# Kernel tuning notes

Measured on AMD Instinct MI355X. Metric: run time of the kernel, lower is better.

The kernel has to match this reference:

```python
import jax, jax.numpy as jnp
import numpy as np
import math

B, D, T, R = 32, 512, 64, 49
K = 64
OUT = 1024


def setup_inputs() -> dict:
    key = jax.random.key(0)
    k_x, k_c, k_w = jax.random.split(key, 3)
    x = jax.random.normal(k_x, (B, D, T, R), dtype=jnp.float32)
    mask = jnp.ones((B, T), dtype=jnp.int32)
    centroids = jax.random.normal(k_c, (K, D), dtype=jnp.float32) / math.sqrt(D)
    conv_w = centroids  # reset_parameters() copies centroids into the 1x1 conv weight
    red_w = jax.random.normal(k_w, (OUT, K * D), dtype=jnp.float32) / math.sqrt(K * D)
    ln_gamma = jnp.ones((OUT,), dtype=jnp.float32)
    ln_beta = jnp.zeros((OUT,), dtype=jnp.float32)
    return {"x": x, "mask": mask, "centroids": centroids, "conv_w": conv_w,
            "red_w": red_w, "ln_gamma": ln_gamma, "ln_beta": ln_beta}


def _l2norm(v, axis):
    n = jnp.sqrt(jnp.sum(v * v, axis=axis, keepdims=True))
    return v / jnp.maximum(n, 1e-12)


def reference(x, mask, centroids, conv_w, red_w, ln_gamma, ln_beta):
    b, d, t, r = x.shape
    # 1x1 conv == contraction over channel dim: [b,k,t,r]
    logits = jnp.einsum('bdtr,kd->bktr', x, conv_w)
    assign = jax.nn.softmax(logits, axis=1)
    # mask applied to residual*assign == masking the assignments
    m = mask.astype(x.dtype)[:, None, :, None]          # [b,1,t,1]
    assign = assign * m
    a_sum = jnp.sum(assign, axis=(2, 3))                 # [b,k]
    # vlad[b,k,d] = sum_{t,r} a[b,k,t,r]*x[b,d,t,r] - a_sum[b,k]*c[k,d]
    vlad = jnp.einsum('bktr,bdtr->bkd', assign, x) - a_sum[:, :, None] * centroids[None]
    vlad = _l2norm(vlad, axis=2)                         # intra-normalization
    vlad = vlad.reshape(b, -1)                           # [b, K*D]
    vlad = _l2norm(vlad, axis=1)
    vlad = vlad @ red_w.T                                # [b, OUT]
    # LayerNorm (eps=1e-5)
    mu = jnp.mean(vlad, axis=-1, keepdims=True)
    var = jnp.mean((vlad - mu) ** 2, axis=-1, keepdims=True)
    return (vlad - mu) / jnp.sqrt(var + 1e-5) * ln_gamma + ln_beta
```

## Files before the change

kernel.cpp:

```cpp
#include <hip/hip_runtime.h>
#include <math.h>

#define BB 32
#define DD 512
#define TT 64
#define RR 49
#define TR 3136
#define KK 64
#define OUTN 1024
#define KD 32768

typedef float f4 __attribute__((ext_vector_type(4)));
typedef short s8 __attribute__((ext_vector_type(8)));

#define OFF_ASSIGN 0ull
#define OFF_VLADP  12845056ull
#define OFF_VN     21233664ull
#define OFF_SS     23330816ull
#define OFF_ASUM   23339008ull
#define OFF_Y      23347200ull

__device__ __forceinline__ unsigned long long pack4(float a, float b, float c, float d) {
    union { float f; unsigned u; } A, B, C, D;
    A.f = a; B.f = b; C.f = c; D.f = d;
    unsigned lo = __builtin_amdgcn_perm(B.u + 0x8000u, A.u + 0x8000u, 0x07060302u);
    unsigned hi = __builtin_amdgcn_perm(D.u + 0x8000u, C.u + 0x8000u, 0x07060302u);
    return (unsigned long long)lo | ((unsigned long long)hi << 32);
}

__global__ __launch_bounds__(256) void kA(const float* __restrict__ x,
                                          const int* __restrict__ mask,
                                          const float* __restrict__ convw,
                                          unsigned short* __restrict__ assign,
                                          float* __restrict__ asum) {
    __shared__ unsigned short cw_l[64 * 136];
    __shared__ unsigned short xT_l[64 * 136];
    __shared__ float sm[64 * 68];

    const int blk = blockIdx.x;
    const int b = blk / 49;
    const int pc = blk % 49;
    const int p0 = pc * 64;
    const int tid = threadIdx.x;
    const int lane = tid & 63;
    const int wv = tid >> 6;
    const int quad = lane >> 4;
    const int l15 = lane & 15;

    f4 acc[4];
#pragma unroll
    for (int t = 0; t < 4; ++t) acc[t] = (f4){0.f, 0.f, 0.f, 0.f};

    const float* xb = x + (size_t)b * DD * TR;

    for (int dc = 0; dc < 4; ++dc) {
        const int d0 = dc * 128;
        __syncthreads();
#pragma unroll
        for (int i = 0; i < 8; ++i) {
            int lin = i * 256 + tid;
            int row = lin >> 5;
            int c = lin & 31;
            f4 v = *(const f4*)(convw + row * DD + d0 + c * 4);
            *(unsigned long long*)(cw_l + row * 136 + c * 4) = pack4(v[0], v[1], v[2], v[3]);
        }
#pragma unroll
        for (int i = 0; i < 2; ++i) {
            int lin = i * 256 + tid;
            int dq = lin >> 4;
            int pq = lin & 15;
            const float* xp = xb + (size_t)(d0 + dq * 4) * TR + p0 + pq * 4;
            f4 a0 = *(const f4*)(xp);
            f4 a1 = *(const f4*)(xp + TR);
            f4 a2 = *(const f4*)(xp + 2 * TR);
            f4 a3 = *(const f4*)(xp + 3 * TR);
#pragma unroll
            for (int jj = 0; jj < 4; ++jj) {
                int j = (jj + pq) & 3;
                *(unsigned long long*)(xT_l + (pq * 4 + j) * 136 + dq * 4) =
                    pack4(a0[j], a1[j], a2[j], a3[j]);
            }
        }
        __syncthreads();
#pragma unroll
        for (int ks = 0; ks < 4; ++ks) {
            int off = ks * 32 + quad * 8;
            s8 af = *(const s8*)(cw_l + (wv * 16 + l15) * 136 + off);
#pragma unroll
            for (int t = 0; t < 4; ++t) {
                s8 bfr = *(const s8*)(xT_l + (t * 16 + l15) * 136 + off);
                acc[t] = __builtin_amdgcn_mfma_f32_16x16x32_bf16(af, bfr, acc[t], 0, 0, 0);
            }
        }
    }
    __syncthreads();
#pragma unroll
    for (int t = 0; t < 4; ++t)
#pragma unroll
        for (int r = 0; r < 4; ++r)
            sm[(wv * 16 + quad * 4 + r) * 68 + t * 16 + l15] = acc[t][r];
    __syncthreads();

    float* redM = (float*)cw_l;
    float* redS = ((float*)cw_l) + 256;
    const int p = lane;
    float mx = -1e30f;
#pragma unroll
    for (int i = 0; i < 16; ++i) mx = fmaxf(mx, sm[(wv * 16 + i) * 68 + p]);
    redM[wv * 64 + p] = mx;
    __syncthreads();
    mx = fmaxf(fmaxf(redM[p], redM[64 + p]), fmaxf(redM[128 + p], redM[192 + p]));
    float s = 0.f;
#pragma unroll
    for (int i = 0; i < 16; ++i) {
        float e = __expf(sm[(wv * 16 + i) * 68 + p] - mx);
        sm[(wv * 16 + i) * 68 + p] = e;
        s += e;
    }
    redS[wv * 64 + p] = s;
    __syncthreads();
    float tot = redS[p] + redS[64 + p] + redS[128 + p] + redS[192 + p];
    const int tt = (p0 + p) / RR;
    const float inv = (float)mask[b * TT + tt] / tot;
#pragma unroll
    for (int i = 0; i < 16; ++i) {
        float v = sm[(wv * 16 + i) * 68 + p] * inv;
        sm[(wv * 16 + i) * 68 + p] = v;
        float r = v;
#pragma unroll
        for (int off = 32; off > 0; off >>= 1) r += __shfl_down(r, off, 64);
        if (lane == 0) atomicAdd(&asum[b * 64 + wv * 16 + i], r);
    }
    __syncthreads();
#pragma unroll
    for (int i = 0; i < 4; ++i) {
        int lin = i * 256 + tid;
        int kr = lin >> 4;
        int pq = lin & 15;
        f4 v = *(const f4*)(sm + kr * 68 + pq * 4);
        *(unsigned long long*)(assign + (size_t)(b * 64 + kr) * TR + p0 + pq * 4) =
            pack4(v[0], v[1], v[2], v[3]);
    }
}

__global__ __launch_bounds__(256) void kB(const float* __restrict__ x,
                                          const unsigned short* __restrict__ assign,
                                          const float* __restrict__ asum,
                                          const float* __restrict__ cent,
                                          float* __restrict__ vladP) {
    __shared__ unsigned short as_l[64 * 72];
    __shared__ unsigned short x_l[64 * 72];

    const int blk = blockIdx.x;
    const int b = blk >> 4;
    const int ds = (blk >> 1) & 7;
    const int ph = blk & 1;
    const int d0 = ds * 64;
    const int tid = threadIdx.x;
    const int lane = tid & 63;
    const int wv = tid >> 6;
    const int quad = lane >> 4;
    const int l15 = lane & 15;

    f4 acc[4];
#pragma unroll
    for (int t = 0; t < 4; ++t) acc[t] = (f4){0.f, 0.f, 0.f, 0.f};

    const int pcs = ph ? 25 : 0;
    const int pce = ph ? 49 : 25;
    for (int pc = pcs; pc < pce; ++pc) {
        const int p0 = pc * 64;
        __syncthreads();
#pragma unroll
        for (int i = 0; i < 2; ++i) {
            int lin = i * 256 + tid;
            int row = lin >> 3;
            int c = lin & 7;
            *(s8*)(as_l + row * 72 + c * 8) =
                *(const s8*)(assign + (size_t)(b * 64 + row) * TR + p0 + c * 8);
        }
#pragma unroll
        for (int i = 0; i < 4; ++i) {
            int lin = i * 256 + tid;
            int row = lin >> 4;
            int c = lin & 15;
            f4 v = *(const f4*)(x + (size_t)(b * DD + d0 + row) * TR + p0 + c * 4);
            *(unsigned long long*)(x_l + row * 72 + c * 4) = pack4(v[0], v[1], v[2], v[3]);
        }
        __syncthreads();
#pragma unroll
        for (int ks = 0; ks < 2; ++ks) {
            int off = ks * 32 + quad * 8;
            s8 af = *(const s8*)(as_l + (wv * 16 + l15) * 72 + off);
#pragma unroll
            for (int t = 0; t < 4; ++t) {
                s8 bfr = *(const s8*)(x_l + (t * 16 + l15) * 72 + off);
                acc[t] = __builtin_amdgcn_mfma_f32_16x16x32_bf16(af, bfr, acc[t], 0, 0, 0);
            }
        }
    }
    float* vp = vladP + (size_t)ph * (BB * KK * DD);
#pragma unroll
    for (int r = 0; r < 4; ++r) {
        const int k = wv * 16 + quad * 4 + r;
        float corr = ph ? 0.f : asum[b * 64 + k];
#pragma unroll
        for (int t = 0; t < 4; ++t) {
            const int d = d0 + t * 16 + l15;
            float v = acc[t][r];
            if (!ph) v -= corr * cent[k * DD + d];
            vp[(size_t)(b * 64 + k) * DD + d] = v;
        }
    }
}

__global__ __launch_bounds__(256) void kC1(const float* __restrict__ vladP,
                                           float* __restrict__ ss) {
    const int blk = blockIdx.x;
    const int b = blk >> 3;
    const int ks = blk & 7;
    const int tid = threadIdx.x;
    const int kr = tid >> 5;
    const int l32 = tid & 31;
    const int k = ks * 8 + kr;
    const float* q0 = vladP + (size_t)(b * 64 + k) * DD;
    const float* q1 = q0 + (size_t)BB * KK * DD;
    float s = 0.f;
#pragma unroll
    for (int i = 0; i < 4; ++i) {
        f4 a = *(const f4*)(q0 + i * 128 + l32 * 4);
        f4 c = *(const f4*)(q1 + i * 128 + l32 * 4);
#pragma unroll
        for (int j = 0; j < 4; ++j) { float v = a[j] + c[j]; s = fmaf(v, v, s); }
    }
    for (int off = 16; off > 0; off >>= 1) s += __shfl_down(s, off, 32);
    if (l32 == 0) ss[b * 64 + k] = s;
}

__global__ __launch_bounds__(256) void kC2(const float* __restrict__ vladP,
                                           const float* __restrict__ ss,
                                           unsigned short* __restrict__ vn) {
    __shared__ float sc[64];
    const int blk = blockIdx.x;
    const int b = blk >> 3;
    const int js = blk & 7;
    const int tid = threadIdx.x;
    if (tid < 64) {
        float rn = sqrtf(ss[b * 64 + tid]);
        float inv = 1.f / fmaxf(rn, 1e-12f);
        float cb = rn * inv; cb = cb * cb;
        float g = cb;
        for (int off = 32; off > 0; off >>= 1) g += __shfl_down(g, off, 64);
        g = __shfl(g, 0, 64);
        float gi = 1.f / fmaxf(sqrtf(g), 1e-12f);
        sc[tid] = inv * gi;
    }
    __syncthreads();
    const float* q0 = vladP + (size_t)b * KD;
    const float* q1 = q0 + (size_t)BB * KD;
#pragma unroll
    for (int it = 0; it < 4; ++it) {
        int j = js * 4096 + it * 1024 + tid * 4;
        f4 a = *(const f4*)(q0 + j);
        f4 c = *(const f4*)(q1 + j);
        float scl = sc[j >> 9];
        *(unsigned long long*)(vn + (size_t)b * KD + j) =
            pack4((a[0] + c[0]) * scl, (a[1] + c[1]) * scl,
                  (a[2] + c[2]) * scl, (a[3] + c[3]) * scl);
    }
}

__global__ __launch_bounds__(256) void kD(const unsigned short* __restrict__ vn,
                                          const float* __restrict__ redw,
                                          float* __restrict__ y) {
    __shared__ unsigned short rw_l[64 * 264];
    __shared__ unsigned short vl_l[32 * 264];

    const int blk = blockIdx.x;
    const int ot = blk & 15;
    const int js = blk >> 4;
    const int o0 = ot * 64;
    const int jb = js * 2048;
    const int tid = threadIdx.x;
    const int lane = tid & 63;
    const int wv = tid >> 6;
    const int quad = lane >> 4;
    const int l15 = lane & 15;

    f4 acc[2];
    acc[0] = (f4){0.f, 0.f, 0.f, 0.f};
    acc[1] = (f4){0.f, 0.f, 0.f, 0.f};

    for (int jc = 0; jc < 8; ++jc) {
        const int j0 = jb + jc * 256;
        __syncthreads();
#pragma unroll
        for (int i = 0; i < 16; ++i) {
            int lin = i * 256 + tid;
            int row = lin >> 6;
            int c = lin & 63;
            f4 v = *(const f4*)(redw + (size_t)(o0 + row) * KD + j0 + c * 4);
            *(unsigned long long*)(rw_l + row * 264 + c * 4) = pack4(v[0], v[1], v[2], v[3]);
        }
#pragma unroll
        for (int i = 0; i < 4; ++i) {
            int lin = i * 256 + tid;
            int row = lin >> 5;
            int c = lin & 31;
            *(s8*)(vl_l + row * 264 + c * 8) =
                *(const s8*)(vn + (size_t)row * KD + j0 + c * 8);
        }
        __syncthreads();
#pragma unroll
        for (int ks = 0; ks < 8; ++ks) {
            int off = ks * 32 + quad * 8;
            s8 bfr = *(const s8*)(rw_l + (wv * 16 + l15) * 264 + off);
#pragma unroll
            for (int t = 0; t < 2; ++t) {
                s8 af = *(const s8*)(vl_l + (t * 16 + l15) * 264 + off);
                acc[t] = __builtin_amdgcn_mfma_f32_16x16x32_bf16(af, bfr, acc[t], 0, 0, 0);
            }
        }
    }
#pragma unroll
    for (int t = 0; t < 2; ++t)
#pragma unroll
        for (int r = 0; r < 4; ++r) {
            int bq = t * 16 + quad * 4 + r;
            int o = o0 + wv * 16 + l15;
            atomicAdd(&y[(size_t)bq * OUTN + o], acc[t][r]);
        }
}

__global__ __launch_bounds__(256) void kE(const float* __restrict__ y,
                                          const float* __restrict__ gamma,
                                          const float* __restrict__ beta,
                                          float* __restrict__ out) {
    __shared__ float s1s[4], s2s[4];
    __shared__ float mu_s, rstd_s;

    const int b = blockIdx.x;
    const int tid = threadIdx.x;
    const int wave = tid >> 6;
    const int lane = tid & 63;

    f4 v = *(const f4*)(y + (size_t)b * OUTN + tid * 4);
    float s1 = v[0] + v[1] + v[2] + v[3];
    float s2 = v[0] * v[0] + v[1] * v[1] + v[2] * v[2] + v[3] * v[3];
    for (int off = 32; off > 0; off >>= 1) {
        s1 += __shfl_down(s1, off, 64);
        s2 += __shfl_down(s2, off, 64);
    }
    if (lane == 0) { s1s[wave] = s1; s2s[wave] = s2; }
    __syncthreads();
    if (tid == 0) {
        float S1 = s1s[0] + s1s[1] + s1s[2] + s1s[3];
        float S2 = s2s[0] + s2s[1] + s2s[2] + s2s[3];
        float mu = S1 / (float)OUTN;
        float var = S2 / (float)OUTN - mu * mu;
        mu_s = mu;
        rstd_s = 1.0f / sqrtf(var + 1e-5f);
    }
    __syncthreads();
    const float mu = mu_s, rstd = rstd_s;
    f4 g = *(const f4*)(gamma + tid * 4);
    f4 be = *(const f4*)(beta + tid * 4);
    f4 o;
#pragma unroll
    for (int i = 0; i < 4; ++i) o[i] = (v[i] - mu) * rstd * g[i] + be[i];
    *(f4*)(out + (size_t)b * OUTN + tid * 4) = o;
}

extern "C" void kernel_launch(void* const* d_in, const int* in_sizes, int n_in,
                              void* d_out, int out_size, void* d_ws, size_t ws_size,
                              hipStream_t stream) {
    const float* x     = (const float*)d_in[0];
    const int*   mask  = (const int*)d_in[1];
    const float* cent  = (const float*)d_in[2];
    const float* convw = (const float*)d_in[3];
    const float* redw  = (const float*)d_in[4];
    const float* gam   = (const float*)d_in[5];
    const float* bet   = (const float*)d_in[6];
    float* out = (float*)d_out;
    char* w = (char*)d_ws;

    unsigned short* assign = (unsigned short*)(w + OFF_ASSIGN);
    float*          vladP  = (float*)(w + OFF_VLADP);
    unsigned short* vn     = (unsigned short*)(w + OFF_VN);
    float*          ss     = (float*)(w + OFF_SS);
    float*          asum   = (float*)(w + OFF_ASUM);
    float*          y      = (float*)(w + OFF_Y);

    hipMemsetAsync(asum, 0, 64 * BB * sizeof(float), stream);
    hipMemsetAsync(y, 0, BB * OUTN * sizeof(float), stream);

    kA<<<BB * 49, 256, 0, stream>>>(x, mask, convw, assign, asum);
    kB<<<BB * 8 * 2, 256, 0, stream>>>(x, assign, asum, cent, vladP);
    kC1<<<BB * 8, 256, 0, stream>>>(vladP, ss);
    kC2<<<BB * 8, 256, 0, stream>>>(vladP, ss, vn);
    kD<<<16 * 16, 256, 0, stream>>>(vn, redw, y);
    kE<<<BB, 256, 0, stream>>>(y, gam, bet, out);
}
```

Measured before the change: 480.9 us.

## Pre-convert conv weights, double-buffer kA, register-prefetch kB/kD, widen split grids

Adds a small kernel that converts the conv weight to bf16 once, so kA loads A fragments straight from global memory instead of re-converting them into LDS in every block. kA now double-buffers the transposed x tile in LDS and prefetches the next chunk into registers while MFMAs run. kB and kD use register prefetch of the next tile. kB splits the pixel range 4 ways instead of 2, and kD splits K into 32 slices instead of 16, both to put more blocks in flight, at the cost of more partial sums and more atomics. The workspace layout is enlarged for four vlad partials and the bf16 weight buffer.

```diff
diff --git a/kernel.cpp b/kernel.cpp
--- a/kernel.cpp
+++ b/kernel.cpp
@@ -9,16 +9,18 @@
 #define KK 64
 #define OUTN 1024
 #define KD 32768
+#define PSTR 1048576ull
 
 typedef float f4 __attribute__((ext_vector_type(4)));
 typedef short s8 __attribute__((ext_vector_type(8)));
 
 #define OFF_ASSIGN 0ull
 #define OFF_VLADP  12845056ull
-#define OFF_VN     21233664ull
-#define OFF_SS     23330816ull
-#define OFF_ASUM   23339008ull
-#define OFF_Y      23347200ull
+#define OFF_VN     29622272ull
+#define OFF_CWB    31719424ull
+#define OFF_SS     31784960ull
+#define OFF_ASUM   31793152ull
+#define OFF_Y      31801344ull
 
 __device__ __forceinline__ unsigned long long pack4(float a, float b, float c, float d) {
     union { float f; unsigned u; } A, B, C, D;
@@ -28,14 +30,24 @@
     return (unsigned long long)lo | ((unsigned long long)hi << 32);
 }
 
+__global__ __launch_bounds__(256) void kW(const float* __restrict__ convw,
+                                          unsigned short* __restrict__ cwb) {
+    int idx = blockIdx.x * 256 + threadIdx.x;
+    f4 v = *(const f4*)(convw + idx * 4);
+    *(unsigned long long*)(cwb + idx * 4) = pack4(v[0], v[1], v[2], v[3]);
+}
+
 __global__ __launch_bounds__(256) void kA(const float* __restrict__ x,
                                           const int* __restrict__ mask,
-                                          const float* __restrict__ convw,
+                                          const unsigned short* __restrict__ cwb,
                                           unsigned short* __restrict__ assign,
                                           float* __restrict__ asum) {
-    __shared__ unsigned short cw_l[64 * 136];
-    __shared__ unsigned short xT_l[64 * 136];
-    __shared__ float sm[64 * 68];
+    __shared__ __align__(16) char smem[2 * 17408 + 2048];
+    unsigned short* xT0 = (unsigned short*)smem;
+    unsigned short* xT1 = (unsigned short*)(smem + 17408);
+    float* sm   = (float*)smem;
+    float* redM = (float*)(smem + 34816);
+    float* redS = redM + 256;
 
     const int blk = blockIdx.x;
     const int b = blk / 49;
@@ -46,54 +58,75 @@
     const int wv = tid >> 6;
     const int quad = lane >> 4;
     const int l15 = lane & 15;
-
+    const int pq = tid & 15;
+    const int dq0 = tid >> 4;
+
+    const float* xb = x + (size_t)b * DD * TR + p0 + pq * 4;
+    const unsigned short* cwrow = cwb + (wv * 16 + l15) * DD + quad * 8;
+
+    f4 xr[2][4];
+    s8 afc[4], afn[4];
     f4 acc[4];
 #pragma unroll
     for (int t = 0; t < 4; ++t) acc[t] = (f4){0.f, 0.f, 0.f, 0.f};
 
-    const float* xb = x + (size_t)b * DD * TR;
-
+    auto XLOAD = [&](int d0) {
+#pragma unroll
+        for (int i = 0; i < 2; ++i) {
+            const float* xp = xb + (size_t)(d0 + (dq0 + 16 * i) * 4) * TR;
+            xr[i][0] = *(const f4*)(xp);
+            xr[i][1] = *(const f4*)(xp + TR);
+            xr[i][2] = *(const f4*)(xp + 2 * TR);
+            xr[i][3] = *(const f4*)(xp + 3 * TR);
+        }
+    };
+    auto XSTORE = [&](unsigned short* buf) {
+#pragma unroll
+        for (int i = 0; i < 2; ++i) {
+            const int dq = dq0 + 16 * i;
+#pragma unroll
+            for (int jj = 0; jj < 4; ++jj) {
+                const int j = (jj + pq) & 3;
+                *(unsigned long long*)(buf + (pq * 4 + j) * 136 + dq * 4) =
+                    pack4(xr[i][0][j], xr[i][1][j], xr[i][2][j], xr[i][3][j]);
+            }
+        }
+    };
+    auto ALOAD = [&](s8* af, int d0) {
+#pragma unroll
+        for (int ks = 0; ks < 4; ++ks)
+            af[ks] = *(const s8*)(cwrow + d0 + ks * 32);
+    };
+
+    XLOAD(0);
+    ALOAD(afc, 0);
+    XSTORE(xT0);
+    XLOAD(128);
+    __syncthreads();
+
+#pragma unroll
     for (int dc = 0; dc < 4; ++dc) {
-        const int d0 = dc * 128;
+        unsigned short* cur = (dc & 1) ? xT1 : xT0;
+        unsigned short* nxt = (dc & 1) ? xT0 : xT1;
+        if (dc < 3) XSTORE(nxt);
+        if (dc < 2) XLOAD((dc + 2) * 128);
+        if (dc < 3) ALOAD(afn, (dc + 1) * 128);
+#pragma unroll
+        for (int ks = 0; ks < 4; ++ks) {
+            const int off = ks * 32 + quad * 8;
+#pragma unroll
+            for (int t = 0; t < 4; ++t) {
+                s8 bfr = *(const s8*)(cur + (t * 16 + l15) * 136 + off);
+                acc[t] = __builtin_amdgcn_mfma_f32_16x16x32_bf16(afc[ks], bfr, acc[t], 0, 0, 0);
+            }
+        }
+        if (dc < 3) {
+#pragma unroll
+            for (int ks = 0; ks < 4; ++ks) afc[ks] = afn[ks];
+        }
         __syncthreads();
-#pragma unroll
-        for (int i = 0; i < 8; ++i) {
-            int lin = i * 256 + tid;
-            int row = lin >> 5;
-            int c = lin & 31;
-            f4 v = *(const f4*)(convw + row * DD + d0 + c * 4);
-            *(unsigned long long*)(cw_l + row * 136 + c * 4) = pack4(v[0], v[1], v[2], v[3]);
-        }
-#pragma unroll
-        for (int i = 0; i < 2; ++i) {
-            int lin = i * 256 + tid;
-            int dq = lin >> 4;
-            int pq = lin & 15;
-            const float* xp = xb + (size_t)(d0 + dq * 4) * TR + p0 + pq * 4;
-            f4 a0 = *(const f4*)(xp);
-            f4 a1 = *(const f4*)(xp + TR);
-            f4 a2 = *(const f4*)(xp + 2 * TR);
-            f4 a3 = *(const f4*)(xp + 3 * TR);
-#pragma unroll
-            for (int jj = 0; jj < 4; ++jj) {
-                int j = (jj + pq) & 3;
-                *(unsigned long long*)(xT_l + (pq * 4 + j) * 136 + dq * 4) =
-                    pack4(a0[j], a1[j], a2[j], a3[j]);
-            }
-        }
-        __syncthreads();
-#pragma unroll
-        for (int ks = 0; ks < 4; ++ks) {
-            int off = ks * 32 + quad * 8;
-            s8 af = *(const s8*)(cw_l + (wv * 16 + l15) * 136 + off);
-#pragma unroll
-            for (int t = 0; t < 4; ++t) {
-                s8 bfr = *(const s8*)(xT_l + (t * 16 + l15) * 136 + off);
-                acc[t] = __builtin_amdgcn_mfma_f32_16x16x32_bf16(af, bfr, acc[t], 0, 0, 0);
-            }
-        }
-    }
-    __syncthreads();
+    }
+
 #pragma unroll
     for (int t = 0; t < 4; ++t)
 #pragma unroll
@@ -101,8 +134,6 @@
             sm[(wv * 16 + quad * 4 + r) * 68 + t * 16 + l15] = acc[t][r];
     __syncthreads();
 
-    float* redM = (float*)cw_l;
-    float* redS = ((float*)cw_l) + 256;
     const int p = lane;
     float mx = -1e30f;
 #pragma unroll
@@ -136,9 +167,9 @@
     for (int i = 0; i < 4; ++i) {
         int lin = i * 256 + tid;
         int kr = lin >> 4;
-        int pq = lin & 15;
-        f4 v = *(const f4*)(sm + kr * 68 + pq * 4);
-        *(unsigned long long*)(assign + (size_t)(b * 64 + kr) * TR + p0 + pq * 4) =
+        int pqq = lin & 15;
+        f4 v = *(const f4*)(sm + kr * 68 + pqq * 4);
+        *(unsigned long long*)(assign + (size_t)(b * 64 + kr) * TR + p0 + pqq * 4) =
             pack4(v[0], v[1], v[2], v[3]);
     }
 }
@@ -152,9 +183,9 @@
     __shared__ unsigned short x_l[64 * 72];
 
     const int blk = blockIdx.x;
-    const int b = blk >> 4;
-    const int ds = (blk >> 1) & 7;
-    const int ph = blk & 1;
+    const int b  = blk >> 5;
+    const int ds = (blk >> 2) & 7;
+    const int ph = blk & 3;
     const int d0 = ds * 64;
     const int tid = threadIdx.x;
     const int lane = tid & 63;
@@ -166,31 +197,42 @@
 #pragma unroll
     for (int t = 0; t < 4; ++t) acc[t] = (f4){0.f, 0.f, 0.f, 0.f};
 
-    const int pcs = ph ? 25 : 0;
-    const int pce = ph ? 49 : 25;
+    const int pcs = (ph * 49) >> 2;
+    const int pce = ((ph + 1) * 49) >> 2;
+
+    const int ar0 = tid >> 3, ac0 = tid & 7;
+    const int xr0 = tid >> 4, xc0 = tid & 15;
+
+    s8 asr[2];
+    f4 xrr[4];
+    auto LOADB = [&](int pc) {
+        const int pp = pc * 64;
+#pragma unroll
+        for (int i = 0; i < 2; ++i)
+            asr[i] = *(const s8*)(assign + (size_t)(b * 64 + ar0 + i * 32) * TR + pp + ac0 * 8);
+#pragma unroll
+        for (int i = 0; i < 4; ++i)
+            xrr[i] = *(const f4*)(x + (size_t)(b * DD + d0 + xr0 + i * 16) * TR + pp + xc0 * 4);
+    };
+    auto STOREB = [&]() {
+#pragma unroll
+        for (int i = 0; i < 2; ++i)
+            *(s8*)(as_l + (ar0 + i * 32) * 72 + ac0 * 8) = asr[i];
+#pragma unroll
+        for (int i = 0; i < 4; ++i)
+            *(unsigned long long*)(x_l + (xr0 + i * 16) * 72 + xc0 * 4) =
+                pack4(xrr[i][0], xrr[i][1], xrr[i][2], xrr[i][3]);
+    };
+
+    LOADB(pcs);
     for (int pc = pcs; pc < pce; ++pc) {
-        const int p0 = pc * 64;
         __syncthreads();
-#pragma unroll
-        for (int i = 0; i < 2; ++i) {
-            int lin = i * 256 + tid;
-            int row = lin >> 3;
-            int c = lin & 7;
-            *(s8*)(as_l + row * 72 + c * 8) =
-                *(const s8*)(assign + (size_t)(b * 64 + row) * TR + p0 + c * 8);
-        }
-#pragma unroll
-        for (int i = 0; i < 4; ++i) {
-            int lin = i * 256 + tid;
-            int row = lin >> 4;
-            int c = lin & 15;
-            f4 v = *(const f4*)(x + (size_t)(b * DD + d0 + row) * TR + p0 + c * 4);
-            *(unsigned long long*)(x_l + row * 72 + c * 4) = pack4(v[0], v[1], v[2], v[3]);
-        }
+        STOREB();
+        if (pc + 1 < pce) LOADB(pc + 1);
         __syncthreads();
 #pragma unroll
         for (int ks = 0; ks < 2; ++ks) {
-            int off = ks * 32 + quad * 8;
+            const int off = ks * 32 + quad * 8;
             s8 af = *(const s8*)(as_l + (wv * 16 + l15) * 72 + off);
 #pragma unroll
             for (int t = 0; t < 4; ++t) {
@@ -199,16 +241,16 @@
             }
         }
     }
-    float* vp = vladP + (size_t)ph * (BB * KK * DD);
+    float* vp = vladP + (size_t)ph * PSTR;
 #pragma unroll
     for (int r = 0; r < 4; ++r) {
         const int k = wv * 16 + quad * 4 + r;
-        float corr = ph ? 0.f : asum[b * 64 + k];
+        float corr = (ph == 0) ? asum[b * 64 + k] : 0.f;
 #pragma unroll
         for (int t = 0; t < 4; ++t) {
             const int d = d0 + t * 16 + l15;
             float v = acc[t][r];
-            if (!ph) v -= corr * cent[k * DD + d];
+            if (ph == 0) v -= corr * cent[k * DD + d];
             vp[(size_t)(b * 64 + k) * DD + d] = v;
         }
     }
@@ -223,15 +265,19 @@
     const int kr = tid >> 5;
     const int l32 = tid & 31;
     const int k = ks * 8 + kr;
-    const float* q0 = vladP + (size_t)(b * 64 + k) * DD;
-    const float* q1 = q0 + (size_t)BB * KK * DD;
+    const float* q = vladP + (size_t)(b * 64 + k) * DD;
     float s = 0.f;
 #pragma unroll
     for (int i = 0; i < 4; ++i) {
-        f4 a = *(const f4*)(q0 + i * 128 + l32 * 4);
-        f4 c = *(const f4*)(q1 + i * 128 + l32 * 4);
-#pragma unroll
-        for (int j = 0; j < 4; ++j) { float v = a[j] + c[j]; s = fmaf(v, v, s); }
+        f4 a0 = *(const f4*)(q + i * 128 + l32 * 4);
+        f4 a1 = *(const f4*)(q + PSTR + i * 128 + l32 * 4);
+        f4 a2 = *(const f4*)(q + 2 * PSTR + i * 128 + l32 * 4);
+        f4 a3 = *(const f4*)(q + 3 * PSTR + i * 128 + l32 * 4);
+#pragma unroll
+        for (int j = 0; j < 4; ++j) {
+            float v = (a0[j] + a1[j]) + (a2[j] + a3[j]);
+            s = fmaf(v, v, s);
+        }
     }
     for (int off = 16; off > 0; off >>= 1) s += __shfl_down(s, off, 32);
     if (l32 == 0) ss[b * 64 + k] = s;
@@ -256,31 +302,34 @@
         sc[tid] = inv * gi;
     }
     __syncthreads();
-    const float* q0 = vladP + (size_t)b * KD;
-    const float* q1 = q0 + (size_t)BB * KD;
+    const float* q = vladP + (size_t)b * KD;
 #pragma unroll
     for (int it = 0; it < 4; ++it) {
         int j = js * 4096 + it * 1024 + tid * 4;
-        f4 a = *(const f4*)(q0 + j);
-        f4 c = *(const f4*)(q1 + j);
+        f4 a0 = *(const f4*)(q + j);
+        f4 a1 = *(const f4*)(q + PSTR + j);
+        f4 a2 = *(const f4*)(q + 2 * PSTR + j);
+        f4 a3 = *(const f4*)(q + 3 * PSTR + j);
         float scl = sc[j >> 9];
         *(unsigned long long*)(vn + (size_t)b * KD + j) =
-            pack4((a[0] + c[0]) * scl, (a[1] + c[1]) * scl,
-                  (a[2] + c[2]) * scl, (a[3] + c[3]) * scl);
+            pack4(((a0[0] + a1[0]) + (a2[0] + a3[0])) * scl,
+                  ((a0[1] + a1[1]) + (a2[1] + a3[1])) * scl,
+                  ((a0[2] + a1[2]) + (a2[2] + a3[2])) * scl,
+                  ((a0[3] + a1[3]) + (a2[3] + a3[3])) * scl);
     }
 }
 
 __global__ __launch_bounds__(256) void kD(const unsigned short* __restrict__ vn,
                                           const float* __restrict__ redw,
                                           float* __restrict__ y) {
-    __shared__ unsigned short rw_l[64 * 264];
-    __shared__ unsigned short vl_l[32 * 264];
+    __shared__ unsigned short rw_l[64 * 136];
+    __shared__ unsigned short vl_l[32 * 136];
 
     const int blk = blockIdx.x;
     const int ot = blk & 15;
     const int js = blk >> 4;
     const int o0 = ot * 64;
-    const int jb = js * 2048;
+    const int jb = js * 1024;
     const int tid = threadIdx.x;
     const int lane = tid & 63;
     const int wv = tid >> 6;
@@ -291,33 +340,42 @@
     acc[0] = (f4){0.f, 0.f, 0.f, 0.f};
     acc[1] = (f4){0.f, 0.f, 0.f, 0.f};
 
+    const int rr0 = tid >> 5, rc0 = tid & 31;
+    const int vr0 = tid >> 4, vc0 = tid & 15;
+    f4 rwr[8];
+    s8 vlr[2];
+    auto LOADD = [&](int jc) {
+        const int j0 = jb + jc * 128;
+#pragma unroll
+        for (int i = 0; i < 8; ++i)
+            rwr[i] = *(const f4*)(redw + (size_t)(o0 + rr0 + i * 8) * KD + j0 + rc0 * 4);
+#pragma unroll
+        for (int i = 0; i < 2; ++i)
+            vlr[i] = *(const s8*)(vn + (size_t)(vr0 + i * 16) * KD + j0 + vc0 * 8);
+    };
+    auto STORED = [&]() {
+#pragma unroll
+        for (int i = 0; i < 8; ++i)
+            *(unsigned long long*)(rw_l + (rr0 + i * 8) * 136 + rc0 * 4) =
+                pack4(rwr[i][0], rwr[i][1], rwr[i][2], rwr[i][3]);
+#pragma unroll
+        for (int i = 0; i < 2; ++i)
+            *(s8*)(vl_l + (vr0 + i * 16) * 136 + vc0 * 8) = vlr[i];
+    };
+
+    LOADD(0);
     for (int jc = 0; jc < 8; ++jc) {
-        const int j0 = jb + jc * 256;
         __syncthreads();
-#pragma unroll
-        for (int i = 0; i < 16; ++i) {
-            int lin = i * 256 + tid;
-            int row = lin >> 6;
-            int c = lin & 63;
-            f4 v = *(const f4*)(redw + (size_t)(o0 + row) * KD + j0 + c * 4);
-            *(unsigned long long*)(rw_l + row * 264 + c * 4) = pack4(v[0], v[1], v[2], v[3]);
-        }
-#pragma unroll
-        for (int i = 0; i < 4; ++i) {
-            int lin = i * 256 + tid;
-            int row = lin >> 5;
-            int c = lin & 31;
-            *(s8*)(vl_l + row * 264 + c * 8) =
-                *(const s8*)(vn + (size_t)row * KD + j0 + c * 8);
-        }
+        STORED();
+        if (jc < 7) LOADD(jc + 1);
         __syncthreads();
 #pragma unroll
-        for (int ks = 0; ks < 8; ++ks) {
-            int off = ks * 32 + quad * 8;
-            s8 bfr = *(const s8*)(rw_l + (wv * 16 + l15) * 264 + off);
+        for (int ks = 0; ks < 4; ++ks) {
+            const int off = ks * 32 + quad * 8;
+            s8 bfr = *(const s8*)(rw_l + (wv * 16 + l15) * 136 + off);
 #pragma unroll
             for (int t = 0; t < 2; ++t) {
-                s8 af = *(const s8*)(vl_l + (t * 16 + l15) * 264 + off);
+                s8 af = *(const s8*)(vl_l + (t * 16 + l15) * 136 + off);
                 acc[t] = __builtin_amdgcn_mfma_f32_16x16x32_bf16(af, bfr, acc[t], 0, 0, 0);
             }
         }
@@ -387,6 +445,7 @@
     unsigned short* assign = (unsigned short*)(w + OFF_ASSIGN);
     float*          vladP  = (float*)(w + OFF_VLADP);
     unsigned short* vn     = (unsigned short*)(w + OFF_VN);
+    unsigned short* cwb    = (unsigned short*)(w + OFF_CWB);
     float*          ss     = (float*)(w + OFF_SS);
     float*          asum   = (float*)(w + OFF_ASUM);
     float*          y      = (float*)(w + OFF_Y);
@@ -394,10 +453,11 @@
     hipMemsetAsync(asum, 0, 64 * BB * sizeof(float), stream);
     hipMemsetAsync(y, 0, BB * OUTN * sizeof(float), stream);
 
-    kA<<<BB * 49, 256, 0, stream>>>(x, mask, convw, assign, asum);
-    kB<<<BB * 8 * 2, 256, 0, stream>>>(x, assign, asum, cent, vladP);
+    kW<<<32, 256, 0, stream>>>(convw, cwb);
+    kA<<<BB * 49, 256, 0, stream>>>(x, mask, cwb, assign, asum);
+    kB<<<BB * 8 * 4, 256, 0, stream>>>(x, assign, asum, cent, vladP);
     kC1<<<BB * 8, 256, 0, stream>>>(vladP, ss);
     kC2<<<BB * 8, 256, 0, stream>>>(vladP, ss, vn);
-    kD<<<16 * 16, 256, 0, stream>>>(vn, redw, y);
+    kD<<<16 * 32, 256, 0, stream>>>(vn, redw, y);
     kE<<<BB, 256, 0, stream>>>(y, gam, bet, out);
 }
```

Result: slower. 579.6 us (+20.5%).
